# Kernel tuning notes

Measured on AMD Instinct MI355X. Metric: run time of the kernel, lower is better.

Reference implementation:

```python
import jax, jax.numpy as jnp
import numpy as np

B, IN_DIM, EMBED_DIM, NUM_TOKENS, CODEBOOK = 4096, 1024, 128, 16, 1024
HID = 512
LATENT = EMBED_DIM * NUM_TOKENS  # 2048


def _lin_init(key, fan_in, fan_out):
    # torch nn.Linear default: U(-1/sqrt(fan_in), 1/sqrt(fan_in))
    kw, kb = jax.random.split(key)
    bound = 1.0 / np.sqrt(fan_in)
    W = jax.random.uniform(kw, (fan_in, fan_out), jnp.float32, -bound, bound)
    b = jax.random.uniform(kb, (fan_out,), jnp.float32, -bound, bound)
    return W, b


def setup_inputs() -> dict:
    key = jax.random.key(0)
    ks = jax.random.split(key, 8)
    x = jax.random.normal(ks[0], (B, IN_DIM), jnp.float32)
    eW1, eb1 = _lin_init(ks[1], IN_DIM, HID)
    eW2, eb2 = _lin_init(ks[2], HID, HID)
    eW3, eb3 = _lin_init(ks[3], HID, LATENT)
    dW1, db1 = _lin_init(ks[4], LATENT, HID)
    dW2, db2 = _lin_init(ks[5], HID, HID)
    dW3, db3 = _lin_init(ks[6], HID, IN_DIM)
    codebook = jax.random.normal(ks[7], (CODEBOOK, EMBED_DIM), jnp.float32)
    return dict(x=x, eW1=eW1, eb1=eb1, eW2=eW2, eb2=eb2, eW3=eW3, eb3=eb3,
                dW1=dW1, db1=db1, dW2=dW2, db2=db2, dW3=dW3, db3=db3,
                codebook=codebook)


def reference(x, eW1, eb1, eW2, eb2, eW3, eb3,
              dW1, db1, dW2, db2, dW3, db3, codebook):
    gelu = lambda t: jax.nn.gelu(t, approximate=False)  # torch GELU is exact
    # encoder MLP
    h = gelu(x @ eW1 + eb1)
    h = gelu(h @ eW2 + eb2)
    z = h @ eW3 + eb3                         # [B, num_tokens*embed_dim]
    z = z.reshape(B * NUM_TOKENS, EMBED_DIM)  # (...) h d flattened
    # VQ: euclidean nearest codebook entry (||z||^2 constant for argmin)
    dist = -2.0 * (z @ codebook.T) + jnp.sum(codebook * codebook, axis=-1)  # [B*T, K]
    indices = jnp.argmin(dist, axis=-1)       # [B*T] int
    quantized = codebook[indices]             # gather [B*T, D]
    commit_loss = jnp.mean((jax.lax.stop_gradient(quantized) - z) ** 2)
    # straight-through estimator
    q = z + jax.lax.stop_gradient(quantized - z)
    q = q.reshape(B, LATENT)
    # decoder MLP
    h = gelu(q @ dW1 + db1)
    h = gelu(h @ dW2 + db2)
    rec = h @ dW3 + db3                       # [B, in_dim]
    return rec, indices.reshape(B, NUM_TOKENS), commit_loss
```

## Files before the change

### kernel.cpp

```cpp
#include <hip/hip_runtime.h>
#include <math.h>

#define BDIM   4096
#define IN_DIM 1024
#define HID    512
#define LAT    2048
#define EMB    128
#define NCODE  1024
#define NROWS  65536
#define OUT_REC  (4096 * 1024)
#define OUT_IDX  (OUT_REC)
#define OUT_LOSS (OUT_REC + 65536)

#define BM 64
#define BN 64
#define BK 16

__device__ __forceinline__ float gelu_exact(float x) {
    return 0.5f * x * (1.0f + erff(x * 0.7071067811865476f));
}

template<bool GELU>
__global__ __launch_bounds__(256) void gemm_bias_kernel(
    const float* __restrict__ A, const float* __restrict__ W,
    const float* __restrict__ bias, float* __restrict__ C,
    int M, int N, int K)
{
    __shared__ float As[BK][BM + 4];
    __shared__ float Ws[BK][BN];

    const int tid = threadIdx.x;
    const int tx = tid & 15, ty = tid >> 4;
    const int bm = blockIdx.x * BM;
    const int bn = blockIdx.y * BN;

    const int a_row = tid >> 2;
    const int a_k   = (tid & 3) * 4;
    const int w_k   = tid >> 4;
    const int w_n   = (tid & 15) * 4;

    const float* Ab = A + (size_t)bm * K;
    const float* Wb = W + bn;

    float acc[4][4] = {};

    for (int k0 = 0; k0 < K; k0 += BK) {
        float4 av = *reinterpret_cast<const float4*>(Ab + (size_t)a_row * K + k0 + a_k);
        float4 wv = *reinterpret_cast<const float4*>(Wb + (size_t)(k0 + w_k) * N + w_n);
        __syncthreads();
        As[a_k + 0][a_row] = av.x;
        As[a_k + 1][a_row] = av.y;
        As[a_k + 2][a_row] = av.z;
        As[a_k + 3][a_row] = av.w;
        *reinterpret_cast<float4*>(&Ws[w_k][w_n]) = wv;
        __syncthreads();
        #pragma unroll
        for (int kk = 0; kk < BK; ++kk) {
            float4 a4 = *reinterpret_cast<const float4*>(&As[kk][ty * 4]);
            float4 w4 = *reinterpret_cast<const float4*>(&Ws[kk][tx * 4]);
            float a_[4] = {a4.x, a4.y, a4.z, a4.w};
            float w_[4] = {w4.x, w4.y, w4.z, w4.w};
            #pragma unroll
            for (int i = 0; i < 4; ++i)
                #pragma unroll
                for (int j = 0; j < 4; ++j)
                    acc[i][j] = fmaf(a_[i], w_[j], acc[i][j]);
        }
    }

    #pragma unroll
    for (int i = 0; i < 4; ++i) {
        const int row = bm + ty * 4 + i;
        #pragma unroll
        for (int j = 0; j < 4; ++j) {
            const int col = bn + tx * 4 + j;
            float v = acc[i][j] + bias[col];
            if (GELU) v = gelu_exact(v);
            C[(size_t)row * N + col] = v;
        }
    }
}

__global__ __launch_bounds__(128) void cnorm_kernel(const float* __restrict__ cb,
                                                    float* __restrict__ cnorm) {
    const int c = blockIdx.x;
    float v = cb[(size_t)c * EMB + threadIdx.x];
    float s = v * v;
    #pragma unroll
    for (int off = 32; off > 0; off >>= 1) s += __shfl_down(s, off, 64);
    __shared__ float ps[2];
    if ((threadIdx.x & 63) == 0) ps[threadIdx.x >> 6] = s;
    __syncthreads();
    if (threadIdx.x == 0) cnorm[c] = ps[0] + ps[1];
}

__global__ __launch_bounds__(256) void vq_kernel(
    float* __restrict__ Z,
    const float* __restrict__ cb,
    const float* __restrict__ cnorm,
    float* __restrict__ idx_out,
    float* __restrict__ loss_accum)
{
    __shared__ float Zs[EMB][BM + 4];
    __shared__ float Cs[EMB][BM + 4];
    __shared__ float red_d[64][17];
    __shared__ int   red_i[64][17];
    __shared__ int   bidx_s[64];
    __shared__ float lred[4];

    const int tid = threadIdx.x;
    const int tx = tid & 15, ty = tid >> 4;
    const int r0 = blockIdx.x * 64;

    const int s_row = tid >> 2;
    const int s_kq  = (tid & 3) * 4;

    #pragma unroll
    for (int kt = 0; kt < 8; ++kt) {
        const int k = kt * 16 + s_kq;
        float4 v = *reinterpret_cast<const float4*>(&Z[(size_t)(r0 + s_row) * EMB + k]);
        Zs[k + 0][s_row] = v.x; Zs[k + 1][s_row] = v.y;
        Zs[k + 2][s_row] = v.z; Zs[k + 3][s_row] = v.w;
    }

    float best[4]; int bidx[4];
    #pragma unroll
    for (int i = 0; i < 4; ++i) { best[i] = 3.4e38f; bidx[i] = 0; }

    for (int cc = 0; cc < 16; ++cc) {
        __syncthreads();
        const int c0 = cc * 64;
        #pragma unroll
        for (int kt = 0; kt < 8; ++kt) {
            const int k = kt * 16 + s_kq;
            float4 v = *reinterpret_cast<const float4*>(&cb[(size_t)(c0 + s_row) * EMB + k]);
            Cs[k + 0][s_row] = v.x; Cs[k + 1][s_row] = v.y;
            Cs[k + 2][s_row] = v.z; Cs[k + 3][s_row] = v.w;
        }
        __syncthreads();

        float acc[4][4] = {};
        #pragma unroll 16
        for (int kk = 0; kk < EMB; ++kk) {
            float4 a4 = *reinterpret_cast<const float4*>(&Zs[kk][ty * 4]);
            float4 c4 = *reinterpret_cast<const float4*>(&Cs[kk][tx * 4]);
            float a_[4] = {a4.x, a4.y, a4.z, a4.w};
            float c_[4] = {c4.x, c4.y, c4.z, c4.w};
            #pragma unroll
            for (int i = 0; i < 4; ++i)
                #pragma unroll
                for (int j = 0; j < 4; ++j)
                    acc[i][j] = fmaf(a_[i], c_[j], acc[i][j]);
        }
        #pragma unroll
        for (int j = 0; j < 4; ++j) {
            const int c = c0 + tx * 4 + j;
            const float cn = cnorm[c];
            #pragma unroll
            for (int i = 0; i < 4; ++i) {
                const float d = cn - 2.0f * acc[i][j];
                if (d < best[i]) { best[i] = d; bidx[i] = c; }
            }
        }
    }

    #pragma unroll
    for (int i = 0; i < 4; ++i) {
        red_d[ty * 4 + i][tx] = best[i];
        red_i[ty * 4 + i][tx] = bidx[i];
    }
    __syncthreads();
    if (tid < 64) {
        float bd = red_d[tid][0]; int bi = red_i[tid][0];
        #pragma unroll
        for (int t = 1; t < 16; ++t) {
            const float d = red_d[tid][t]; const int ii = red_i[tid][t];
            if (d < bd || (d == bd && ii < bi)) { bd = d; bi = ii; }
        }
        idx_out[r0 + tid] = (float)bi;
        bidx_s[tid] = bi;
    }
    __syncthreads();

    float lsum = 0.0f;
    #pragma unroll
    for (int p = 0; p < 32; ++p) {
        const int el = tid + p * 256;
        const int row = el >> 7, k = el & 127;
        const float qv = cb[(size_t)bidx_s[row] * EMB + k];
        const float zv = Zs[k][row];
        const float dv = qv - zv;
        lsum += dv * dv;
        Z[(size_t)(r0 + row) * EMB + k] = qv;
    }
    #pragma unroll
    for (int off = 32; off > 0; off >>= 1) lsum += __shfl_down(lsum, off, 64);
    if ((tid & 63) == 0) lred[tid >> 6] = lsum;
    __syncthreads();
    if (tid == 0) atomicAdd(loss_accum, lred[0] + lred[1] + lred[2] + lred[3]);
}

__global__ void loss_fin_kernel(const float* __restrict__ acc, float* __restrict__ out) {
    out[0] = acc[0] * (1.0f / 8388608.0f);
}

extern "C" void kernel_launch(void* const* d_in, const int* in_sizes, int n_in,
                              void* d_out, int out_size, void* d_ws, size_t ws_size,
                              hipStream_t stream) {
    const float* x   = (const float*)d_in[0];
    const float* eW1 = (const float*)d_in[1];
    const float* eb1 = (const float*)d_in[2];
    const float* eW2 = (const float*)d_in[3];
    const float* eb2 = (const float*)d_in[4];
    const float* eW3 = (const float*)d_in[5];
    const float* eb3 = (const float*)d_in[6];
    const float* dW1 = (const float*)d_in[7];
    const float* db1 = (const float*)d_in[8];
    const float* dW2 = (const float*)d_in[9];
    const float* db2 = (const float*)d_in[10];
    const float* dW3 = (const float*)d_in[11];
    const float* db3 = (const float*)d_in[12];
    const float* cb  = (const float*)d_in[13];

    float* out = (float*)d_out;
    float* ws  = (float*)d_ws;

    float* h1    = ws;
    float* h2    = h1 + (size_t)BDIM * HID;
    float* z     = h2 + (size_t)BDIM * HID;
    float* cnorm = z + (size_t)BDIM * LAT;
    float* lacc  = cnorm + NCODE;

    hipMemsetAsync(lacc, 0, sizeof(float), stream);
    cnorm_kernel<<<NCODE, 128, 0, stream>>>(cb, cnorm);

    gemm_bias_kernel<true ><<<dim3(BDIM / BM, HID / BN), 256, 0, stream>>>(x,  eW1, eb1, h1, BDIM, HID, IN_DIM);
    gemm_bias_kernel<true ><<<dim3(BDIM / BM, HID / BN), 256, 0, stream>>>(h1, eW2, eb2, h2, BDIM, HID, HID);
    gemm_bias_kernel<false><<<dim3(BDIM / BM, LAT / BN), 256, 0, stream>>>(h2, eW3, eb3, z,  BDIM, LAT, HID);

    vq_kernel<<<NROWS / 64, 256, 0, stream>>>(z, cb, cnorm, out + OUT_IDX, lacc);

    gemm_bias_kernel<true ><<<dim3(BDIM / BM, HID / BN),    256, 0, stream>>>(z,  dW1, db1, h1, BDIM, HID, LAT);
    gemm_bias_kernel<true ><<<dim3(BDIM / BM, HID / BN),    256, 0, stream>>>(h1, dW2, db2, h2, BDIM, HID, HID);
    gemm_bias_kernel<false><<<dim3(BDIM / BM, IN_DIM / BN), 256, 0, stream>>>(h2, dW3, db3, out, BDIM, IN_DIM, HID);

    loss_fin_kernel<<<1, 1, 0, stream>>>(lacc, out + OUT_LOSS);
}
```

Measured before the change: 782.8 us.

## Use split-bf16 MFMA GEMMs for decoder and retile VQ distance kernel

The decoder GEMMs now run on MFMA bf16 instructions, with each fp32 operand split into hi and lo bf16 parts (three MFMAs per tile) to keep near-fp32 accuracy. Decoder weights are pre-transposed and split by new prep kernels, and the VQ kernel writes the quantized rows in the packed hi/lo format the next GEMM reads. The VQ distance kernel uses a transposed codebook, an 8x8 per-thread register tile and a shuffle-based argmin reduction instead of the shared-memory one. This targets the scalar FMA cost of the decoder and VQ stages, at the price of extra prep kernels each call and a small precision loss from the bf16 split.

```diff
diff --git a/kernel.cpp b/kernel.cpp
--- a/kernel.cpp
+++ b/kernel.cpp
@@ -1,4 +1,5 @@
 #include <hip/hip_runtime.h>
+#include <hip/hip_bf16.h>
 #include <math.h>
 
 #define BDIM   4096
@@ -12,12 +13,28 @@
 #define OUT_IDX  (OUT_REC)
 #define OUT_LOSS (OUT_REC + 65536)
 
-#define BM 64
-#define BN 64
-#define BK 16
+#define H1_OFF    0u
+#define H2_OFF    (2u*1024*1024)
+#define Z_OFF     (4u*1024*1024)
+#define CBT_OFF   (12u*1024*1024)
+#define CNORM_OFF (CBT_OFF + 131072u)
+#define LACC_OFF  (CNORM_OFF + 1024u)
+#define WT_OFF    (LACC_OFF + 8u)
+
+typedef __attribute__((ext_vector_type(8))) __bf16 bf16x8;
+typedef __attribute__((ext_vector_type(4))) float f32x4;
+typedef __attribute__((ext_vector_type(8))) unsigned short u16x8;
 
 __device__ __forceinline__ float gelu_exact(float x) {
     return 0.5f * x * (1.0f + erff(x * 0.7071067811865476f));
+}
+
+__device__ __forceinline__ void split_bf16(float v, unsigned short& hi, unsigned short& lo) {
+    __hip_bfloat16 h = __float2bfloat16(v);
+    float hf = __bfloat162float(h);
+    __hip_bfloat16 l = __float2bfloat16(v - hf);
+    hi = *reinterpret_cast<unsigned short*>(&h);
+    lo = *reinterpret_cast<unsigned short*>(&l);
 }
 
 template<bool GELU>
@@ -26,36 +43,27 @@
     const float* __restrict__ bias, float* __restrict__ C,
     int M, int N, int K)
 {
-    __shared__ float As[BK][BM + 4];
-    __shared__ float Ws[BK][BN];
-
+    __shared__ float As[16][64 + 4];
+    __shared__ float Ws[16][64];
     const int tid = threadIdx.x;
     const int tx = tid & 15, ty = tid >> 4;
-    const int bm = blockIdx.x * BM;
-    const int bn = blockIdx.y * BN;
-
-    const int a_row = tid >> 2;
-    const int a_k   = (tid & 3) * 4;
-    const int w_k   = tid >> 4;
-    const int w_n   = (tid & 15) * 4;
-
+    const int bm = blockIdx.x * 64;
+    const int bn = blockIdx.y * 64;
+    const int a_row = tid >> 2, a_k = (tid & 3) * 4;
+    const int w_k = tid >> 4, w_n = (tid & 15) * 4;
     const float* Ab = A + (size_t)bm * K;
     const float* Wb = W + bn;
-
     float acc[4][4] = {};
-
-    for (int k0 = 0; k0 < K; k0 += BK) {
+    for (int k0 = 0; k0 < K; k0 += 16) {
         float4 av = *reinterpret_cast<const float4*>(Ab + (size_t)a_row * K + k0 + a_k);
         float4 wv = *reinterpret_cast<const float4*>(Wb + (size_t)(k0 + w_k) * N + w_n);
         __syncthreads();
-        As[a_k + 0][a_row] = av.x;
-        As[a_k + 1][a_row] = av.y;
-        As[a_k + 2][a_row] = av.z;
-        As[a_k + 3][a_row] = av.w;
+        As[a_k + 0][a_row] = av.x; As[a_k + 1][a_row] = av.y;
+        As[a_k + 2][a_row] = av.z; As[a_k + 3][a_row] = av.w;
         *reinterpret_cast<float4*>(&Ws[w_k][w_n]) = wv;
         __syncthreads();
         #pragma unroll
-        for (int kk = 0; kk < BK; ++kk) {
+        for (int kk = 0; kk < 16; ++kk) {
             float4 a4 = *reinterpret_cast<const float4*>(&As[kk][ty * 4]);
             float4 w4 = *reinterpret_cast<const float4*>(&Ws[kk][tx * 4]);
             float a_[4] = {a4.x, a4.y, a4.z, a4.w};
@@ -67,7 +75,6 @@
                     acc[i][j] = fmaf(a_[i], w_[j], acc[i][j]);
         }
     }
-
     #pragma unroll
     for (int i = 0; i < 4; ++i) {
         const int row = bm + ty * 4 + i;
@@ -94,110 +101,247 @@
     if (threadIdx.x == 0) cnorm[c] = ps[0] + ps[1];
 }
 
-__global__ __launch_bounds__(256) void vq_kernel(
-    float* __restrict__ Z,
-    const float* __restrict__ cb,
+__global__ __launch_bounds__(256) void transpose_f32_kernel(const float* __restrict__ in,
+        float* __restrict__ out, int R, int C) {
+    __shared__ float tile[32][33];
+    const int r0 = blockIdx.y * 32, c0 = blockIdx.x * 32;
+    const int tx = threadIdx.x, ty = threadIdx.y;
+    #pragma unroll
+    for (int i = 0; i < 4; ++i)
+        tile[ty * 4 + i][tx] = in[(size_t)(r0 + ty * 4 + i) * C + c0 + tx];
+    __syncthreads();
+    #pragma unroll
+    for (int i = 0; i < 4; ++i)
+        out[(size_t)(c0 + ty * 4 + i) * R + r0 + tx] = tile[tx][ty * 4 + i];
+}
+
+__global__ __launch_bounds__(256) void wsplitT_kernel(const float* __restrict__ W,
+        unsigned short* __restrict__ hiT, unsigned short* __restrict__ loT, int K, int N) {
+    __shared__ float tile[32][33];
+    const int k0 = blockIdx.y * 32, n0 = blockIdx.x * 32;
+    const int tx = threadIdx.x, ty = threadIdx.y;
+    #pragma unroll
+    for (int i = 0; i < 4; ++i)
+        tile[ty * 4 + i][tx] = W[(size_t)(k0 + ty * 4 + i) * N + n0 + tx];
+    __syncthreads();
+    #pragma unroll
+    for (int i = 0; i < 4; ++i) {
+        float v = tile[tx][ty * 4 + i];
+        unsigned short h, l; split_bf16(v, h, l);
+        size_t o = (size_t)(n0 + ty * 4 + i) * K + k0 + tx;
+        hiT[o] = h; loT[o] = l;
+    }
+}
+
+__global__ __launch_bounds__(256) void vq2_kernel(
+    const float* __restrict__ Z, unsigned short* __restrict__ qpack,
+    const float* __restrict__ cbT, const float* __restrict__ cb,
     const float* __restrict__ cnorm,
-    float* __restrict__ idx_out,
-    float* __restrict__ loss_accum)
+    float* __restrict__ idx_out, float* __restrict__ loss_accum)
 {
-    __shared__ float Zs[EMB][BM + 4];
-    __shared__ float Cs[EMB][BM + 4];
-    __shared__ float red_d[64][17];
-    __shared__ int   red_i[64][17];
-    __shared__ int   bidx_s[64];
+    __shared__ float Zs[128][68];
+    __shared__ float Cs[32][260];
+    __shared__ int bidx_s[64];
     __shared__ float lred[4];
-
     const int tid = threadIdx.x;
-    const int tx = tid & 15, ty = tid >> 4;
+    const int tx = tid & 31, ty = tid >> 5;
     const int r0 = blockIdx.x * 64;
 
-    const int s_row = tid >> 2;
-    const int s_kq  = (tid & 3) * 4;
-
-    #pragma unroll
-    for (int kt = 0; kt < 8; ++kt) {
-        const int k = kt * 16 + s_kq;
-        float4 v = *reinterpret_cast<const float4*>(&Z[(size_t)(r0 + s_row) * EMB + k]);
-        Zs[k + 0][s_row] = v.x; Zs[k + 1][s_row] = v.y;
-        Zs[k + 2][s_row] = v.z; Zs[k + 3][s_row] = v.w;
-    }
-
-    float best[4]; int bidx[4];
-    #pragma unroll
-    for (int i = 0; i < 4; ++i) { best[i] = 3.4e38f; bidx[i] = 0; }
-
-    for (int cc = 0; cc < 16; ++cc) {
-        __syncthreads();
-        const int c0 = cc * 64;
-        #pragma unroll
-        for (int kt = 0; kt < 8; ++kt) {
-            const int k = kt * 16 + s_kq;
-            float4 v = *reinterpret_cast<const float4*>(&cb[(size_t)(c0 + s_row) * EMB + k]);
-            Cs[k + 0][s_row] = v.x; Cs[k + 1][s_row] = v.y;
-            Cs[k + 2][s_row] = v.z; Cs[k + 3][s_row] = v.w;
-        }
-        __syncthreads();
-
-        float acc[4][4] = {};
-        #pragma unroll 16
-        for (int kk = 0; kk < EMB; ++kk) {
-            float4 a4 = *reinterpret_cast<const float4*>(&Zs[kk][ty * 4]);
-            float4 c4 = *reinterpret_cast<const float4*>(&Cs[kk][tx * 4]);
-            float a_[4] = {a4.x, a4.y, a4.z, a4.w};
-            float c_[4] = {c4.x, c4.y, c4.z, c4.w};
-            #pragma unroll
-            for (int i = 0; i < 4; ++i)
+    #pragma unroll
+    for (int p = 0; p < 8; ++p) {
+        int s = tid + p * 256;
+        int row = s >> 5, k4 = (s & 31) * 4;
+        float4 v = *reinterpret_cast<const float4*>(&Z[(size_t)(r0 + row) * EMB + k4]);
+        Zs[k4 + 0][row] = v.x; Zs[k4 + 1][row] = v.y;
+        Zs[k4 + 2][row] = v.z; Zs[k4 + 3][row] = v.w;
+    }
+
+    float best[8]; int bidx[8];
+    #pragma unroll
+    for (int i = 0; i < 8; ++i) { best[i] = 3.4e38f; bidx[i] = 0; }
+
+    for (int cc = 0; cc < 4; ++cc) {
+        float acc[8][8] = {};
+        for (int kc = 0; kc < 4; ++kc) {
+            __syncthreads();
+            #pragma unroll
+            for (int p = 0; p < 8; ++p) {
+                int s = tid + p * 256;
+                int kr = s >> 6, c4 = (s & 63) * 4;
+                float4 v = *reinterpret_cast<const float4*>(
+                    &cbT[(size_t)(kc * 32 + kr) * NCODE + cc * 256 + c4]);
+                *reinterpret_cast<float4*>(&Cs[kr][c4]) = v;
+            }
+            __syncthreads();
+            #pragma unroll
+            for (int kk = 0; kk < 32; ++kk) {
+                f32x4 a0 = *reinterpret_cast<const f32x4*>(&Zs[kc * 32 + kk][ty * 8]);
+                f32x4 a1 = *reinterpret_cast<const f32x4*>(&Zs[kc * 32 + kk][ty * 8 + 4]);
+                f32x4 c0 = *reinterpret_cast<const f32x4*>(&Cs[kk][tx * 8]);
+                f32x4 c1 = *reinterpret_cast<const f32x4*>(&Cs[kk][tx * 8 + 4]);
+                float a[8] = {a0.x, a0.y, a0.z, a0.w, a1.x, a1.y, a1.z, a1.w};
+                float c[8] = {c0.x, c0.y, c0.z, c0.w, c1.x, c1.y, c1.z, c1.w};
                 #pragma unroll
-                for (int j = 0; j < 4; ++j)
-                    acc[i][j] = fmaf(a_[i], c_[j], acc[i][j]);
-        }
-        #pragma unroll
-        for (int j = 0; j < 4; ++j) {
-            const int c = c0 + tx * 4 + j;
-            const float cn = cnorm[c];
-            #pragma unroll
-            for (int i = 0; i < 4; ++i) {
-                const float d = cn - 2.0f * acc[i][j];
+                for (int i = 0; i < 8; ++i)
+                    #pragma unroll
+                    for (int j = 0; j < 8; ++j)
+                        acc[i][j] = fmaf(a[i], c[j], acc[i][j]);
+            }
+        }
+        #pragma unroll
+        for (int j = 0; j < 8; ++j) {
+            int c = cc * 256 + tx * 8 + j;
+            float cn = cnorm[c];
+            #pragma unroll
+            for (int i = 0; i < 8; ++i) {
+                float d = cn - 2.0f * acc[i][j];
                 if (d < best[i]) { best[i] = d; bidx[i] = c; }
             }
         }
     }
-
-    #pragma unroll
-    for (int i = 0; i < 4; ++i) {
-        red_d[ty * 4 + i][tx] = best[i];
-        red_i[ty * 4 + i][tx] = bidx[i];
+    #pragma unroll
+    for (int i = 0; i < 8; ++i) {
+        float bd = best[i]; int bi = bidx[i];
+        #pragma unroll
+        for (int m = 1; m < 32; m <<= 1) {
+            float od = __shfl_xor(bd, m); int oi = __shfl_xor(bi, m);
+            if (od < bd || (od == bd && oi < bi)) { bd = od; bi = oi; }
+        }
+        if (tx == 0) {
+            int row = ty * 8 + i;
+            idx_out[r0 + row] = (float)bi;
+            bidx_s[row] = bi;
+        }
     }
     __syncthreads();
-    if (tid < 64) {
-        float bd = red_d[tid][0]; int bi = red_i[tid][0];
-        #pragma unroll
-        for (int t = 1; t < 16; ++t) {
-            const float d = red_d[tid][t]; const int ii = red_i[tid][t];
-            if (d < bd || (d == bd && ii < bi)) { bd = d; bi = ii; }
-        }
-        idx_out[r0 + tid] = (float)bi;
-        bidx_s[tid] = bi;
-    }
-    __syncthreads();
-
     float lsum = 0.0f;
     #pragma unroll
     for (int p = 0; p < 32; ++p) {
-        const int el = tid + p * 256;
-        const int row = el >> 7, k = el & 127;
-        const float qv = cb[(size_t)bidx_s[row] * EMB + k];
-        const float zv = Zs[k][row];
-        const float dv = qv - zv;
+        int el = p * 256 + tid;
+        int row = el >> 7, k = el & 127;
+        int bi = bidx_s[row];
+        float qv = cb[(size_t)bi * EMB + k];
+        float zv = Zs[k][row];
+        float dv = qv - zv;
         lsum += dv * dv;
-        Z[(size_t)(r0 + row) * EMB + k] = qv;
+        unsigned short h, l; split_bf16(qv, h, l);
+        size_t base = (size_t)(r0 + row) * 256;
+        qpack[base + k] = h;
+        qpack[base + 128 + k] = l;
     }
     #pragma unroll
     for (int off = 32; off > 0; off >>= 1) lsum += __shfl_down(lsum, off, 64);
     if ((tid & 63) == 0) lred[tid >> 6] = lsum;
     __syncthreads();
     if (tid == 0) atomicAdd(loss_accum, lred[0] + lred[1] + lred[2] + lred[3]);
+}
+
+template<int AMODE, bool GELU, int OMODE>
+__global__ __launch_bounds__(256) void mfma_gemm_kernel(
+    const unsigned short* __restrict__ Ahi, const unsigned short* __restrict__ Alo,
+    const unsigned short* __restrict__ BThi, const unsigned short* __restrict__ BTlo,
+    const float* __restrict__ bias,
+    float* __restrict__ Cf, unsigned short* __restrict__ Ohi, unsigned short* __restrict__ Olo,
+    int M, int N, int K)
+{
+    __shared__ unsigned short AsH[128][40], AsL[128][40], BsH[128][40], BsL[128][40];
+    const int tid = threadIdx.x;
+    const int lane = tid & 63, wid = tid >> 6;
+    const int wm = (wid >> 1) * 64, wn = (wid & 1) * 64;
+    const int m0 = blockIdx.x * 128, n0 = blockIdx.y * 128;
+
+    f32x4 acc[4][4];
+    #pragma unroll
+    for (int i = 0; i < 4; ++i)
+        #pragma unroll
+        for (int j = 0; j < 4; ++j)
+            acc[i][j] = f32x4{0.f, 0.f, 0.f, 0.f};
+
+    const int ar0 = tid >> 1;
+    const int s0 = tid, s1 = tid + 256;
+    const int r0_ = s0 >> 2, k0_ = (s0 & 3) * 8;
+    const int r1_ = s1 >> 2, k1_ = (s1 & 3) * 8;
+    (void)ar0;
+
+    for (int k0 = 0; k0 < K; k0 += 32) {
+        u16x8 vA0, vA1, vAl0, vAl1, vB0, vB1, vBl0, vBl1;
+        if (AMODE == 1) {
+            int kk0 = k0 + k0_, kk1 = k0 + k1_;
+            size_t g0 = ((size_t)(m0 + r0_) * 16 + (kk0 >> 7)) * 256 + (kk0 & 127);
+            size_t g1 = ((size_t)(m0 + r1_) * 16 + (kk1 >> 7)) * 256 + (kk1 & 127);
+            vA0  = *reinterpret_cast<const u16x8*>(Ahi + g0);
+            vAl0 = *reinterpret_cast<const u16x8*>(Ahi + g0 + 128);
+            vA1  = *reinterpret_cast<const u16x8*>(Ahi + g1);
+            vAl1 = *reinterpret_cast<const u16x8*>(Ahi + g1 + 128);
+        } else {
+            size_t g0 = (size_t)(m0 + r0_) * K + k0 + k0_;
+            size_t g1 = (size_t)(m0 + r1_) * K + k0 + k1_;
+            vA0  = *reinterpret_cast<const u16x8*>(Ahi + g0);
+            vAl0 = *reinterpret_cast<const u16x8*>(Alo + g0);
+            vA1  = *reinterpret_cast<const u16x8*>(Ahi + g1);
+            vAl1 = *reinterpret_cast<const u16x8*>(Alo + g1);
+        }
+        {
+            size_t g0 = (size_t)(n0 + r0_) * K + k0 + k0_;
+            size_t g1 = (size_t)(n0 + r1_) * K + k0 + k1_;
+            vB0  = *reinterpret_cast<const u16x8*>(BThi + g0);
+            vBl0 = *reinterpret_cast<const u16x8*>(BTlo + g0);
+            vB1  = *reinterpret_cast<const u16x8*>(BThi + g1);
+            vBl1 = *reinterpret_cast<const u16x8*>(BTlo + g1);
+        }
+        __syncthreads();
+        *reinterpret_cast<u16x8*>(&AsH[r0_][k0_]) = vA0;
+        *reinterpret_cast<u16x8*>(&AsH[r1_][k1_]) = vA1;
+        *reinterpret_cast<u16x8*>(&AsL[r0_][k0_]) = vAl0;
+        *reinterpret_cast<u16x8*>(&AsL[r1_][k1_]) = vAl1;
+        *reinterpret_cast<u16x8*>(&BsH[r0_][k0_]) = vB0;
+        *reinterpret_cast<u16x8*>(&BsH[r1_][k1_]) = vB1;
+        *reinterpret_cast<u16x8*>(&BsL[r0_][k0_]) = vBl0;
+        *reinterpret_cast<u16x8*>(&BsL[r1_][k1_]) = vBl1;
+        __syncthreads();
+
+        const int fr = lane & 15, fk = (lane >> 4) * 8;
+        bf16x8 ah[4], al[4];
+        #pragma unroll
+        for (int mi = 0; mi < 4; ++mi) {
+            ah[mi] = *reinterpret_cast<const bf16x8*>(&AsH[wm + mi * 16 + fr][fk]);
+            al[mi] = *reinterpret_cast<const bf16x8*>(&AsL[wm + mi * 16 + fr][fk]);
+        }
+        #pragma unroll
+        for (int ni = 0; ni < 4; ++ni) {
+            bf16x8 bh = *reinterpret_cast<const bf16x8*>(&BsH[wn + ni * 16 + fr][fk]);
+            bf16x8 bl = *reinterpret_cast<const bf16x8*>(&BsL[wn + ni * 16 + fr][fk]);
+            #pragma unroll
+            for (int mi = 0; mi < 4; ++mi) {
+                acc[mi][ni] = __builtin_amdgcn_mfma_f32_16x16x32_bf16(ah[mi], bh, acc[mi][ni], 0, 0, 0);
+                acc[mi][ni] = __builtin_amdgcn_mfma_f32_16x16x32_bf16(ah[mi], bl, acc[mi][ni], 0, 0, 0);
+                acc[mi][ni] = __builtin_amdgcn_mfma_f32_16x16x32_bf16(al[mi], bh, acc[mi][ni], 0, 0, 0);
+            }
+        }
+    }
+
+    const int fr = lane & 15, fq = lane >> 4;
+    #pragma unroll
+    for (int ni = 0; ni < 4; ++ni) {
+        int col = n0 + wn + ni * 16 + fr;
+        float bv = bias[col];
+        #pragma unroll
+        for (int mi = 0; mi < 4; ++mi) {
+            #pragma unroll
+            for (int r = 0; r < 4; ++r) {
+                int row = m0 + wm + mi * 16 + fq * 4 + r;
+                float v = acc[mi][ni][r] + bv;
+                if (GELU) v = gelu_exact(v);
+                if (OMODE == 0) {
+                    Cf[(size_t)row * N + col] = v;
+                } else {
+                    unsigned short h, l; split_bf16(v, h, l);
+                    Ohi[(size_t)row * N + col] = h;
+                    Olo[(size_t)row * N + col] = l;
+                }
+            }
+        }
+    }
 }
 
 __global__ void loss_fin_kernel(const float* __restrict__ acc, float* __restrict__ out) {
@@ -225,24 +369,45 @@
     float* out = (float*)d_out;
     float* ws  = (float*)d_ws;
 
-    float* h1    = ws;
-    float* h2    = h1 + (size_t)BDIM * HID;
-    float* z     = h2 + (size_t)BDIM * HID;
-    float* cnorm = z + (size_t)BDIM * LAT;
-    float* lacc  = cnorm + NCODE;
+    float* h1    = ws + H1_OFF;
+    float* h2    = ws + H2_OFF;
+    float* z     = ws + Z_OFF;
+    float* cbT   = ws + CBT_OFF;
+    float* cnorm = ws + CNORM_OFF;
+    float* lacc  = ws + LACC_OFF;
+
+    unsigned short* qpack = (unsigned short*)z;
+    unsigned short* h1hi = (unsigned short*)h1;
+    unsigned short* h1lo = (unsigned short*)(h1 + 1048576);
+    unsigned short* h2hi = (unsigned short*)h2;
+    unsigned short* h2lo = (unsigned short*)(h2 + 1048576);
+    unsigned short* wt   = (unsigned short*)(ws + WT_OFF);
+    unsigned short* W1TH = wt;
+    unsigned short* W1TL = wt + 1048576u;
+    unsigned short* W2TH = wt + 2097152u;
+    unsigned short* W2TL = wt + 2359296u;
+    unsigned short* W3TH = wt + 2621440u;
+    unsigned short* W3TL = wt + 3145728u;
 
     hipMemsetAsync(lacc, 0, sizeof(float), stream);
     cnorm_kernel<<<NCODE, 128, 0, stream>>>(cb, cnorm);
-
-    gemm_bias_kernel<true ><<<dim3(BDIM / BM, HID / BN), 256, 0, stream>>>(x,  eW1, eb1, h1, BDIM, HID, IN_DIM);
-    gemm_bias_kernel<true ><<<dim3(BDIM / BM, HID / BN), 256, 0, stream>>>(h1, eW2, eb2, h2, BDIM, HID, HID);
-    gemm_bias_kernel<false><<<dim3(BDIM / BM, LAT / BN), 256, 0, stream>>>(h2, eW3, eb3, z,  BDIM, LAT, HID);
-
-    vq_kernel<<<NROWS / 64, 256, 0, stream>>>(z, cb, cnorm, out + OUT_IDX, lacc);
-
-    gemm_bias_kernel<true ><<<dim3(BDIM / BM, HID / BN),    256, 0, stream>>>(z,  dW1, db1, h1, BDIM, HID, LAT);
-    gemm_bias_kernel<true ><<<dim3(BDIM / BM, HID / BN),    256, 0, stream>>>(h1, dW2, db2, h2, BDIM, HID, HID);
-    gemm_bias_kernel<false><<<dim3(BDIM / BM, IN_DIM / BN), 256, 0, stream>>>(h2, dW3, db3, out, BDIM, IN_DIM, HID);
+    transpose_f32_kernel<<<dim3(EMB / 32, NCODE / 32), dim3(32, 8), 0, stream>>>(cb, cbT, NCODE, EMB);
+    wsplitT_kernel<<<dim3(HID / 32, LAT / 32),    dim3(32, 8), 0, stream>>>(dW1, W1TH, W1TL, LAT, HID);
+    wsplitT_kernel<<<dim3(HID / 32, HID / 32),    dim3(32, 8), 0, stream>>>(dW2, W2TH, W2TL, HID, HID);
+    wsplitT_kernel<<<dim3(IN_DIM / 32, HID / 32), dim3(32, 8), 0, stream>>>(dW3, W3TH, W3TL, HID, IN_DIM);
+
+    gemm_bias_kernel<true ><<<dim3(BDIM / 64, HID / 64), 256, 0, stream>>>(x,  eW1, eb1, h1, BDIM, HID, IN_DIM);
+    gemm_bias_kernel<true ><<<dim3(BDIM / 64, HID / 64), 256, 0, stream>>>(h1, eW2, eb2, h2, BDIM, HID, HID);
+    gemm_bias_kernel<false><<<dim3(BDIM / 64, LAT / 64), 256, 0, stream>>>(h2, eW3, eb3, z,  BDIM, LAT, HID);
+
+    vq2_kernel<<<NROWS / 64, 256, 0, stream>>>(z, qpack, cbT, cb, cnorm, out + OUT_IDX, lacc);
+
+    mfma_gemm_kernel<1, true, 1><<<dim3(BDIM / 128, HID / 128), 256, 0, stream>>>(
+        qpack, nullptr, W1TH, W1TL, db1, nullptr, h1hi, h1lo, BDIM, HID, LAT);
+    mfma_gemm_kernel<0, true, 1><<<dim3(BDIM / 128, HID / 128), 256, 0, stream>>>(
+        h1hi, h1lo, W2TH, W2TL, db2, nullptr, h2hi, h2lo, BDIM, HID, HID);
+    mfma_gemm_kernel<0, false, 0><<<dim3(BDIM / 128, IN_DIM / 128), 256, 0, stream>>>(
+        h2hi, h2lo, W3TH, W3TL, db3, out, nullptr, nullptr, BDIM, IN_DIM, HID);
 
     loss_fin_kernel<<<1, 1, 0, stream>>>(lacc, out + OUT_LOSS);
 }
```

New measurement: 772.6 us. About the same (-1.3%).
